# Optimization experiments

Measured on AMD Instinct MI355X. Metric: run time of the kernel, lower is better.

## Reference

```python
import jax, jax.numpy as jnp
import numpy as np

N, E, F, H = 50000, 800000, 128, 128
EPS = 1e-5


def _layernorm(x, gamma, beta):
    mu = jnp.mean(x, axis=-1, keepdims=True)
    var = jnp.mean(jnp.square(x - mu), axis=-1, keepdims=True)
    return (x - mu) * jax.lax.rsqrt(var + EPS) * gamma + beta


def setup_inputs() -> dict:
    key = jax.random.key(0)
    ks = jax.random.split(key, 12)
    x = jax.random.normal(ks[0], (N, F), dtype=jnp.float32)
    edge_idx = jax.random.randint(ks[1], (2, E), 0, N, dtype=jnp.int64)
    edge_attr = jax.random.normal(ks[2], (E, H), dtype=jnp.float32)
    u = jax.random.normal(ks[3], (N, H), dtype=jnp.float32)
    # node_mlp_1 params: Linear(F+H -> H), Linear(H -> H), LayerNorm(H)
    W1a = jax.random.normal(ks[4], (F + H, H), dtype=jnp.float32) / np.sqrt(F + H)
    b1a = jnp.zeros((H,), jnp.float32)
    W2a = jax.random.normal(ks[5], (H, H), dtype=jnp.float32) / np.sqrt(H)
    b2a = jnp.zeros((H,), jnp.float32)
    g1 = jnp.ones((H,), jnp.float32)
    be1 = jnp.zeros((H,), jnp.float32)
    # node_mlp_2 params: Linear(F+2H -> H), Linear(H -> H), LayerNorm(H)
    W1b = jax.random.normal(ks[6], (F + 2 * H, H), dtype=jnp.float32) / np.sqrt(F + 2 * H)
    b1b = jnp.zeros((H,), jnp.float32)
    W2b = jax.random.normal(ks[7], (H, H), dtype=jnp.float32) / np.sqrt(H)
    b2b = jnp.zeros((H,), jnp.float32)
    g2 = jnp.ones((H,), jnp.float32)
    be2 = jnp.zeros((H,), jnp.float32)
    return dict(x=x, edge_idx=edge_idx, edge_attr=edge_attr, u=u,
                W1a=W1a, b1a=b1a, W2a=W2a, b2a=b2a, g1=g1, be1=be1,
                W1b=W1b, b1b=b1b, W2b=W2b, b2b=b2b, g2=g2, be2=be2)


def reference(x, edge_idx, edge_attr, u,
              W1a, b1a, W2a, b2a, g1, be1,
              W1b, b1b, W2b, b2b, g2, be2):
    row, col = edge_idx[0], edge_idx[1]
    # gather source nodes, concat with edge features -> [E, F+H]
    msg = jnp.concatenate([x[col], edge_attr], axis=1)
    h = jax.nn.relu(msg @ W1a + b1a)
    h = _layernorm(h @ W2a + b2a, g1, be1)  # [E, H]
    # scatter_mean over destination nodes
    summed = jax.ops.segment_sum(h, row, num_segments=x.shape[0])
    counts = jax.ops.segment_sum(jnp.ones((h.shape[0],), h.dtype), row,
                                 num_segments=x.shape[0])
    agg = summed / jnp.clip(counts, 1.0)[:, None]  # [N, H]
    z = jnp.concatenate([x, agg, u], axis=1)  # [N, F+2H]
    z = jax.nn.relu(z @ W1b + b1b)
    return _layernorm(z @ W2b + b2b, g2, be2)  # [N, H]
```

## Files before the change

kernel.cpp:

```cpp
#include <hip/hip_runtime.h>
#include <hip/hip_fp16.h>


typedef __bf16 bf16x8 __attribute__((ext_vector_type(8)));
typedef float floatx4 __attribute__((ext_vector_type(4)));

__device__ __forceinline__ unsigned short f2bf(float f) {
    unsigned int u = __float_as_uint(f);
    u = u + 0x7FFFu + ((u >> 16) & 1u);
    return (unsigned short)(u >> 16);
}
__device__ __forceinline__ unsigned int pk2(float a, float b) {
    return (unsigned int)f2bf(a) | ((unsigned int)f2bf(b) << 16);
}

__global__ void detect_idx64(const unsigned int* __restrict__ idx, int* __restrict__ flag) {
    if (threadIdx.x == 0 && blockIdx.x == 0) {
        unsigned int o = 0;
        for (int i = 1; i < 64; i += 2) o |= idx[i];
        *flag = (o == 0u) ? 1 : 0;
    }
}

__global__ void prep_weights(const float* __restrict__ W1a, const float* __restrict__ W2a,
                             const float* __restrict__ W1b, const float* __restrict__ W2b,
                             unsigned short* __restrict__ w1aT, unsigned short* __restrict__ w2aT,
                             unsigned short* __restrict__ w1bT, unsigned short* __restrict__ w2bT) {
    int g = blockIdx.x * 256 + threadIdx.x;
    if (g < 32768) {
        int n = g >> 8, k = g & 255;
        w1aT[g] = f2bf(W1a[k * 128 + n]);
    } else if (g < 49152) {
        int l = g - 32768; int n = l >> 7, k = l & 127;
        w2aT[l] = f2bf(W2a[k * 128 + n]);
    } else if (g < 98304) {
        int l = g - 49152; int n = l / 384, k = l - n * 384;
        w1bT[l] = f2bf(W1b[k * 128 + n]);
    } else if (g < 114688) {
        int l = g - 98304; int n = l >> 7, k = l & 127;
        w2bT[l] = f2bf(W2b[k * 128 + n]);
    }
}

__global__ __launch_bounds__(256, 2) void edge_mlp_scatter(
    const float* __restrict__ x, const void* __restrict__ eidx,
    const float* __restrict__ ea,
    const float* __restrict__ b1a, const float* __restrict__ b2a,
    const float* __restrict__ g1, const float* __restrict__ be1,
    const unsigned short* __restrict__ w1aT, const unsigned short* __restrict__ w2aT,
    float* __restrict__ summed, __half* __restrict__ summedH,
    float* __restrict__ counts,
    const int* __restrict__ flag64, int E, int useHalf)
{
    __shared__ union {
        unsigned short msg[64 * 264];
        float h2[64 * 132];
    } uA;
    __shared__ unsigned short h1s[64 * 136];
    __shared__ int lsRow[64], lsCol[64];
    __shared__ float sMean[64], sRstd[64];

    const int tid  = threadIdx.x;
    const int lane = tid & 63;
    const int wave = tid >> 6;
    const int quad = lane >> 4;
    const int lm   = lane & 15;
    const int ns   = wave * 32;

    bf16x8 wf1[8][2], wf2[4][2];
#pragma unroll
    for (int kk = 0; kk < 8; kk++)
#pragma unroll
        for (int nt = 0; nt < 2; nt++)
            wf1[kk][nt] = *(const bf16x8*)(w1aT + (ns + nt * 16 + lm) * 256 + kk * 32 + quad * 8);
#pragma unroll
    for (int kk = 0; kk < 4; kk++)
#pragma unroll
        for (int nt = 0; nt < 2; nt++)
            wf2[kk][nt] = *(const bf16x8*)(w2aT + (ns + nt * 16 + lm) * 128 + kk * 32 + quad * 8);

    float b1v[2], b2v[2];
#pragma unroll
    for (int nt = 0; nt < 2; nt++) {
        b1v[nt] = b1a[ns + nt * 16 + lm];
        b2v[nt] = b2a[ns + nt * 16 + lm];
    }
    const int colT = tid & 127;
    const float gv = g1[colT], bev = be1[colT];
    const int colP = tid & 63, eg4 = tid >> 6;
    float gA = 0.f, gB = 0.f, bA = 0.f, bB = 0.f;
    if (useHalf) {
        gA = g1[colP * 2];  gB = g1[colP * 2 + 1];
        bA = be1[colP * 2]; bB = be1[colP * 2 + 1];
    }
    const int use64 = *flag64;

    const int numTiles = (E + 63) >> 6;
    for (int t = blockIdx.x; t < numTiles; t += gridDim.x) {
        const int eb = t << 6;
        __syncthreads();
        if (tid < 64) {
            int e = eb + tid; if (e >= E) e = E - 1;
            int r, c;
            if (use64) { const long long* p = (const long long*)eidx; r = (int)p[e]; c = (int)p[E + e]; }
            else       { const int* p = (const int*)eidx;             r = p[e];      c = p[E + e]; }
            lsRow[tid] = r; lsCol[tid] = c;
        }
        __syncthreads();
        {
            const int rl = tid >> 5, l32 = tid & 31;
#pragma unroll
            for (int it = 0; it < 8; it++) {
                const int e = it * 8 + rl;
                int eg = eb + e; if (eg >= E) eg = E - 1;
                const float4 xv = ((const float4*)(x + (size_t)lsCol[e] * 128))[l32];
                const float4 av = ((const float4*)(ea + (size_t)eg * 128))[l32];
                *(unsigned int*)&uA.msg[e * 264 + l32 * 4]           = pk2(xv.x, xv.y);
                *(unsigned int*)&uA.msg[e * 264 + l32 * 4 + 2]       = pk2(xv.z, xv.w);
                *(unsigned int*)&uA.msg[e * 264 + 128 + l32 * 4]     = pk2(av.x, av.y);
                *(unsigned int*)&uA.msg[e * 264 + 128 + l32 * 4 + 2] = pk2(av.z, av.w);
            }
        }
        __syncthreads();
        floatx4 acc1[4][2] = {};
#pragma unroll
        for (int mt = 0; mt < 4; mt++)
#pragma unroll
            for (int kk = 0; kk < 8; kk++) {
                bf16x8 a = *(const bf16x8*)&uA.msg[(mt * 16 + lm) * 264 + kk * 32 + quad * 8];
                acc1[mt][0] = __builtin_amdgcn_mfma_f32_16x16x32_bf16(a, wf1[kk][0], acc1[mt][0], 0, 0, 0);
                acc1[mt][1] = __builtin_amdgcn_mfma_f32_16x16x32_bf16(a, wf1[kk][1], acc1[mt][1], 0, 0, 0);
            }
#pragma unroll
        for (int mt = 0; mt < 4; mt++)
#pragma unroll
            for (int nt = 0; nt < 2; nt++)
#pragma unroll
                for (int r = 0; r < 4; r++) {
                    const int row = mt * 16 + quad * 4 + r;
                    const int col = ns + nt * 16 + lm;
                    h1s[row * 136 + col] = f2bf(fmaxf(acc1[mt][nt][r] + b1v[nt], 0.f));
                }
        __syncthreads();
        floatx4 acc2[4][2] = {};
#pragma unroll
        for (int mt = 0; mt < 4; mt++)
#pragma unroll
            for (int kk = 0; kk < 4; kk++) {
                bf16x8 a = *(const bf16x8*)&h1s[(mt * 16 + lm) * 136 + kk * 32 + quad * 8];
                acc2[mt][0] = __builtin_amdgcn_mfma_f32_16x16x32_bf16(a, wf2[kk][0], acc2[mt][0], 0, 0, 0);
                acc2[mt][1] = __builtin_amdgcn_mfma_f32_16x16x32_bf16(a, wf2[kk][1], acc2[mt][1], 0, 0, 0);
            }
#pragma unroll
        for (int mt = 0; mt < 4; mt++)
#pragma unroll
            for (int nt = 0; nt < 2; nt++)
#pragma unroll
                for (int r = 0; r < 4; r++) {
                    const int row = mt * 16 + quad * 4 + r;
                    const int col = ns + nt * 16 + lm;
                    uA.h2[row * 132 + col] = acc2[mt][nt][r] + b2v[nt];
                }
        __syncthreads();
        {
            const int e = tid >> 2, q = tid & 3;
            const float4* hp = (const float4*)&uA.h2[e * 132 + q * 32];
            float s = 0.f, ss = 0.f;
#pragma unroll
            for (int i = 0; i < 8; i++) {
                float4 v = hp[i];
                s  += v.x + v.y + v.z + v.w;
                ss += v.x * v.x + v.y * v.y + v.z * v.z + v.w * v.w;
            }
            s  += __shfl_xor(s, 1);  s  += __shfl_xor(s, 2);
            ss += __shfl_xor(ss, 1); ss += __shfl_xor(ss, 2);
            if (q == 0) {
                float mean = s * (1.f / 128.f);
                float var  = ss * (1.f / 128.f) - mean * mean;
                sMean[e] = mean;
                sRstd[e] = rsqrtf(var + 1e-5f);
                if (eb + e < E) unsafeAtomicAdd(counts + lsRow[e], 1.f);
            }
        }
        __syncthreads();
        if (useHalf) {
#pragma unroll
            for (int it = 0; it < 16; it++) {
                const int e = it * 4 + eg4;
                if (eb + e < E) {
                    const float2 h = *(const float2*)&uA.h2[e * 132 + colP * 2];
                    const float m = sMean[e], rs = sRstd[e];
                    const float v0 = (h.x - m) * rs * gA + bA;
                    const float v1 = (h.y - m) * rs * gB + bB;
                    unsafeAtomicAdd((__half2*)(summedH + (size_t)lsRow[e] * 128 + colP * 2),
                                    __floats2half2_rn(v0, v1));
                }
            }
        } else {
#pragma unroll
            for (int it = 0; it < 32; it++) {
                const int e = it * 2 + (tid >> 7);
                if (eb + e < E) {
                    float v = (uA.h2[e * 132 + colT] - sMean[e]) * sRstd[e] * gv + bev;
                    unsafeAtomicAdd(summed + (size_t)lsRow[e] * 128 + colT, v);
                }
            }
        }
    }
}

__global__ __launch_bounds__(256, 2) void node_mlp(
    const float* __restrict__ x, const float* __restrict__ u,
    const float* summed, const __half* __restrict__ summedH,
    const float* __restrict__ counts,
    const float* __restrict__ b1b, const float* __restrict__ b2b,
    const float* __restrict__ g2, const float* __restrict__ be2,
    const unsigned short* __restrict__ w1bT, const unsigned short* __restrict__ w2bT,
    float* out, int NN, int useHalf)
{
    __shared__ union {
        unsigned short msg[32 * 392];
        float h2[32 * 132];
    } uA;
    __shared__ unsigned short h1s[32 * 136];
    __shared__ float sMean[32], sRstd[32];

    const int tid  = threadIdx.x;
    const int lane = tid & 63;
    const int wave = tid >> 6;
    const int quad = lane >> 4;
    const int lm   = lane & 15;
    const int ns   = wave * 32;

    bf16x8 wf1[12][2], wf2[4][2];
#pragma unroll
    for (int kk = 0; kk < 12; kk++)
#pragma unroll
        for (int nt = 0; nt < 2; nt++)
            wf1[kk][nt] = *(const bf16x8*)(w1bT + (ns + nt * 16 + lm) * 384 + kk * 32 + quad * 8);
#pragma unroll
    for (int kk = 0; kk < 4; kk++)
#pragma unroll
        for (int nt = 0; nt < 2; nt++)
            wf2[kk][nt] = *(const bf16x8*)(w2bT + (ns + nt * 16 + lm) * 128 + kk * 32 + quad * 8);

    float b1v[2], b2v[2];
#pragma unroll
    for (int nt = 0; nt < 2; nt++) {
        b1v[nt] = b1b[ns + nt * 16 + lm];
        b2v[nt] = b2b[ns + nt * 16 + lm];
    }
    const int colT = tid & 127;
    const float gv = g2[colT], bev = be2[colT];

    const int numTiles = (NN + 31) >> 5;
    for (int t = blockIdx.x; t < numTiles; t += gridDim.x) {
        const int nb = t << 5;
        __syncthreads();
        {
            const int rl = tid >> 5, l32 = tid & 31;
#pragma unroll
            for (int it = 0; it < 4; it++) {
                const int rloc = it * 8 + rl;
                int i = nb + rloc; if (i >= NN) i = NN - 1;
                const float4 xv = ((const float4*)(x + (size_t)i * 128))[l32];
                float4 sv;
                if (useHalf) {
                    const float2 rw = ((const float2*)(summedH + (size_t)i * 128))[l32];
                    const __half2 h01 = *(const __half2*)&rw.x;
                    const __half2 h23 = *(const __half2*)&rw.y;
                    const float2 a = __half22float2(h01);
                    const float2 b = __half22float2(h23);
                    sv.x = a.x; sv.y = a.y; sv.z = b.x; sv.w = b.y;
                } else {
                    sv = ((const float4*)(summed + (size_t)i * 128))[l32];
                }
                const float inv = 1.f / fmaxf(counts[i], 1.f);
                sv.x *= inv; sv.y *= inv; sv.z *= inv; sv.w *= inv;
                const float4 uv = ((const float4*)(u + (size_t)i * 128))[l32];
                *(unsigned int*)&uA.msg[rloc * 392 + l32 * 4]           = pk2(xv.x, xv.y);
                *(unsigned int*)&uA.msg[rloc * 392 + l32 * 4 + 2]       = pk2(xv.z, xv.w);
                *(unsigned int*)&uA.msg[rloc * 392 + 128 + l32 * 4]     = pk2(sv.x, sv.y);
                *(unsigned int*)&uA.msg[rloc * 392 + 128 + l32 * 4 + 2] = pk2(sv.z, sv.w);
                *(unsigned int*)&uA.msg[rloc * 392 + 256 + l32 * 4]     = pk2(uv.x, uv.y);
                *(unsigned int*)&uA.msg[rloc * 392 + 256 + l32 * 4 + 2] = pk2(uv.z, uv.w);
            }
        }
        __syncthreads();
        floatx4 acc1[2][2] = {};
#pragma unroll
        for (int mt = 0; mt < 2; mt++)
#pragma unroll
            for (int kk = 0; kk < 12; kk++) {
                bf16x8 a = *(const bf16x8*)&uA.msg[(mt * 16 + lm) * 392 + kk * 32 + quad * 8];
                acc1[mt][0] = __builtin_amdgcn_mfma_f32_16x16x32_bf16(a, wf1[kk][0], acc1[mt][0], 0, 0, 0);
                acc1[mt][1] = __builtin_amdgcn_mfma_f32_16x16x32_bf16(a, wf1[kk][1], acc1[mt][1], 0, 0, 0);
            }
#pragma unroll
        for (int mt = 0; mt < 2; mt++)
#pragma unroll
            for (int nt = 0; nt < 2; nt++)
#pragma unroll
                for (int r = 0; r < 4; r++) {
                    const int row = mt * 16 + quad * 4 + r;
                    const int col = ns + nt * 16 + lm;
                    h1s[row * 136 + col] = f2bf(fmaxf(acc1[mt][nt][r] + b1v[nt], 0.f));
                }
        __syncthreads();
        floatx4 acc2[2][2] = {};
#pragma unroll
        for (int mt = 0; mt < 2; mt++)
#pragma unroll
            for (int kk = 0; kk < 4; kk++) {
                bf16x8 a = *(const bf16x8*)&h1s[(mt * 16 + lm) * 136 + kk * 32 + quad * 8];
                acc2[mt][0] = __builtin_amdgcn_mfma_f32_16x16x32_bf16(a, wf2[kk][0], acc2[mt][0], 0, 0, 0);
                acc2[mt][1] = __builtin_amdgcn_mfma_f32_16x16x32_bf16(a, wf2[kk][1], acc2[mt][1], 0, 0, 0);
            }
#pragma unroll
        for (int mt = 0; mt < 2; mt++)
#pragma unroll
            for (int nt = 0; nt < 2; nt++)
#pragma unroll
                for (int r = 0; r < 4; r++) {
                    const int row = mt * 16 + quad * 4 + r;
                    const int col = ns + nt * 16 + lm;
                    uA.h2[row * 132 + col] = acc2[mt][nt][r] + b2v[nt];
                }
        __syncthreads();
        {
            const int e = tid >> 3, q = tid & 7;
            const float4* hp = (const float4*)&uA.h2[e * 132 + q * 16];
            float s = 0.f, ss = 0.f;
#pragma unroll
            for (int i = 0; i < 4; i++) {
                float4 v = hp[i];
                s  += v.x + v.y + v.z + v.w;
                ss += v.x * v.x + v.y * v.y + v.z * v.z + v.w * v.w;
            }
            s  += __shfl_xor(s, 1);  s  += __shfl_xor(s, 2);  s  += __shfl_xor(s, 4);
            ss += __shfl_xor(ss, 1); ss += __shfl_xor(ss, 2); ss += __shfl_xor(ss, 4);
            if (q == 0) {
                float mean = s * (1.f / 128.f);
                float var  = ss * (1.f / 128.f) - mean * mean;
                sMean[e] = mean;
                sRstd[e] = rsqrtf(var + 1e-5f);
            }
        }
        __syncthreads();
        {
            const int half = tid >> 7;
#pragma unroll
            for (int it = 0; it < 16; it++) {
                const int rloc = it * 2 + half;
                const int i = nb + rloc;
                if (i < NN) {
                    float v = (uA.h2[rloc * 132 + colT] - sMean[rloc]) * sRstd[rloc] * gv + bev;
                    out[(size_t)i * 128 + colT] = v;
                }
            }
        }
    }
}

extern "C" void kernel_launch(void* const* d_in, const int* in_sizes, int n_in,
                              void* d_out, int out_size, void* d_ws, size_t ws_size,
                              hipStream_t stream)
{
    const float* x   = (const float*)d_in[0];
    const void*  eidx = d_in[1];
    const float* ea  = (const float*)d_in[2];
    const float* u   = (const float*)d_in[3];
    const float* W1a = (const float*)d_in[4];
    const float* b1a = (const float*)d_in[5];
    const float* W2a = (const float*)d_in[6];
    const float* b2a = (const float*)d_in[7];
    const float* g1  = (const float*)d_in[8];
    const float* be1 = (const float*)d_in[9];
    const float* W1b = (const float*)d_in[10];
    const float* b1b = (const float*)d_in[11];
    const float* W2b = (const float*)d_in[12];
    const float* b2b = (const float*)d_in[13];
    const float* g2  = (const float*)d_in[14];
    const float* be2 = (const float*)d_in[15];

    const int NN = in_sizes[0] / 128;
    const int E  = in_sizes[2] / 128;

    float* counts = (float*)d_ws;
    int*   flag   = (int*)((char*)d_ws + (size_t)NN * 4);
    size_t woff   = (((size_t)NN * 4 + 4) + 15) & ~(size_t)15;
    unsigned short* w1aT = (unsigned short*)((char*)d_ws + woff);
    unsigned short* w2aT = w1aT + 128 * 256;
    unsigned short* w1bT = w2aT + 128 * 128;
    unsigned short* w2bT = w1bT + 128 * 384;
    size_t shoff  = (woff + (size_t)(128*256 + 128*128 + 128*384 + 128*128) * 2 + 255) & ~(size_t)255;
    __half* summedH = (__half*)((char*)d_ws + shoff);
    const int useHalf = (ws_size >= shoff + (size_t)NN * 128 * 2) ? 1 : 0;

    float* outf = (float*)d_out;

    if (useHalf) {
        hipMemsetAsync(summedH, 0, (size_t)NN * 128 * 2, stream);
    } else {
        hipMemsetAsync(d_out, 0, (size_t)out_size * 4, stream);
    }
    hipMemsetAsync(counts, 0, (size_t)NN * 4, stream);
    detect_idx64<<<1, 64, 0, stream>>>((const unsigned int*)eidx, flag);
    prep_weights<<<448, 256, 0, stream>>>(W1a, W2a, W1b, W2b, w1aT, w2aT, w1bT, w2bT);

    edge_mlp_scatter<<<512, 256, 0, stream>>>(x, eidx, ea, b1a, b2a, g1, be1,
                                              w1aT, w2aT, outf, summedH, counts, flag, E, useHalf);

    node_mlp<<<512, 256, 0, stream>>>(x, u, outf, summedH, counts, b1b, b2b, g2, be2,
                                      w1bT, w2bT, outf, NN, useHalf);
}
```

Before: 795.6 us.

## Double block size to 512 threads with 16 output columns per wave

Both the edge and node MLP kernels now run 512-thread blocks (8 waves), and each wave owns 16 output columns instead of 32. This halves the per-wave weight fragments and accumulators held in registers, which allows more resident waves per CU and more latency hiding for the gather and atomic scatter. The gather, layernorm reduction and scatter loops are re-indexed for the larger block. In exchange, each A-tile read from shared memory now feeds only one MFMA instead of two, so LDS traffic per MFMA doubles, and there are more waves per barrier.

```diff
diff --git a/kernel.cpp b/kernel.cpp
--- a/kernel.cpp
+++ b/kernel.cpp
@@ -42,7 +42,7 @@
     }
 }
 
-__global__ __launch_bounds__(256, 2) void edge_mlp_scatter(
+__global__ __launch_bounds__(512, 4) void edge_mlp_scatter(
     const float* __restrict__ x, const void* __restrict__ eidx,
     const float* __restrict__ ea,
     const float* __restrict__ b1a, const float* __restrict__ b2a,
@@ -65,29 +65,21 @@
     const int wave = tid >> 6;
     const int quad = lane >> 4;
     const int lm   = lane & 15;
-    const int ns   = wave * 32;
-
-    bf16x8 wf1[8][2], wf2[4][2];
+    const int ns   = wave * 16;
+
+    bf16x8 wf1[8], wf2[4];
 #pragma unroll
     for (int kk = 0; kk < 8; kk++)
-#pragma unroll
-        for (int nt = 0; nt < 2; nt++)
-            wf1[kk][nt] = *(const bf16x8*)(w1aT + (ns + nt * 16 + lm) * 256 + kk * 32 + quad * 8);
+        wf1[kk] = *(const bf16x8*)(w1aT + (ns + lm) * 256 + kk * 32 + quad * 8);
 #pragma unroll
     for (int kk = 0; kk < 4; kk++)
-#pragma unroll
-        for (int nt = 0; nt < 2; nt++)
-            wf2[kk][nt] = *(const bf16x8*)(w2aT + (ns + nt * 16 + lm) * 128 + kk * 32 + quad * 8);
-
-    float b1v[2], b2v[2];
-#pragma unroll
-    for (int nt = 0; nt < 2; nt++) {
-        b1v[nt] = b1a[ns + nt * 16 + lm];
-        b2v[nt] = b2a[ns + nt * 16 + lm];
-    }
+        wf2[kk] = *(const bf16x8*)(w2aT + (ns + lm) * 128 + kk * 32 + quad * 8);
+
+    const float b1v = b1a[ns + lm];
+    const float b2v = b2a[ns + lm];
     const int colT = tid & 127;
     const float gv = g1[colT], bev = be1[colT];
-    const int colP = tid & 63, eg4 = tid >> 6;
+    const int colP = tid & 63;
     float gA = 0.f, gB = 0.f, bA = 0.f, bB = 0.f;
     if (useHalf) {
         gA = g1[colP * 2];  gB = g1[colP * 2 + 1];
@@ -110,8 +102,8 @@
         {
             const int rl = tid >> 5, l32 = tid & 31;
 #pragma unroll
-            for (int it = 0; it < 8; it++) {
-                const int e = it * 8 + rl;
+            for (int it = 0; it < 4; it++) {
+                const int e = it * 16 + rl;
                 int eg = eb + e; if (eg >= E) eg = E - 1;
                 const float4 xv = ((const float4*)(x + (size_t)lsCol[e] * 128))[l32];
                 const float4 av = ((const float4*)(ea + (size_t)eg * 128))[l32];
@@ -122,58 +114,50 @@
             }
         }
         __syncthreads();
-        floatx4 acc1[4][2] = {};
+        floatx4 acc1[4] = {};
 #pragma unroll
         for (int mt = 0; mt < 4; mt++)
 #pragma unroll
             for (int kk = 0; kk < 8; kk++) {
                 bf16x8 a = *(const bf16x8*)&uA.msg[(mt * 16 + lm) * 264 + kk * 32 + quad * 8];
-                acc1[mt][0] = __builtin_amdgcn_mfma_f32_16x16x32_bf16(a, wf1[kk][0], acc1[mt][0], 0, 0, 0);
-                acc1[mt][1] = __builtin_amdgcn_mfma_f32_16x16x32_bf16(a, wf1[kk][1], acc1[mt][1], 0, 0, 0);
+                acc1[mt] = __builtin_amdgcn_mfma_f32_16x16x32_bf16(a, wf1[kk], acc1[mt], 0, 0, 0);
             }
 #pragma unroll
         for (int mt = 0; mt < 4; mt++)
 #pragma unroll
-            for (int nt = 0; nt < 2; nt++)
-#pragma unroll
-                for (int r = 0; r < 4; r++) {
-                    const int row = mt * 16 + quad * 4 + r;
-                    const int col = ns + nt * 16 + lm;
-                    h1s[row * 136 + col] = f2bf(fmaxf(acc1[mt][nt][r] + b1v[nt], 0.f));
-                }
-        __syncthreads();
-        floatx4 acc2[4][2] = {};
+            for (int r = 0; r < 4; r++) {
+                const int row = mt * 16 + quad * 4 + r;
+                h1s[row * 136 + ns + lm] = f2bf(fmaxf(acc1[mt][r] + b1v, 0.f));
+            }
+        __syncthreads();
+        floatx4 acc2[4] = {};
 #pragma unroll
         for (int mt = 0; mt < 4; mt++)
 #pragma unroll
             for (int kk = 0; kk < 4; kk++) {
                 bf16x8 a = *(const bf16x8*)&h1s[(mt * 16 + lm) * 136 + kk * 32 + quad * 8];
-                acc2[mt][0] = __builtin_amdgcn_mfma_f32_16x16x32_bf16(a, wf2[kk][0], acc2[mt][0], 0, 0, 0);
-                acc2[mt][1] = __builtin_amdgcn_mfma_f32_16x16x32_bf16(a, wf2[kk][1], acc2[mt][1], 0, 0, 0);
+                acc2[mt] = __builtin_amdgcn_mfma_f32_16x16x32_bf16(a, wf2[kk], acc2[mt], 0, 0, 0);
             }
 #pragma unroll
         for (int mt = 0; mt < 4; mt++)
 #pragma unroll
-            for (int nt = 0; nt < 2; nt++)
-#pragma unroll
-                for (int r = 0; r < 4; r++) {
-                    const int row = mt * 16 + quad * 4 + r;
-                    const int col = ns + nt * 16 + lm;
-                    uA.h2[row * 132 + col] = acc2[mt][nt][r] + b2v[nt];
-                }
-        __syncthreads();
-        {
-            const int e = tid >> 2, q = tid & 3;
-            const float4* hp = (const float4*)&uA.h2[e * 132 + q * 32];
+            for (int r = 0; r < 4; r++) {
+                const int row = mt * 16 + quad * 4 + r;
+                uA.h2[row * 132 + ns + lm] = acc2[mt][r] + b2v;
+            }
+        __syncthreads();
+        {
+            const int e = tid >> 3, q = tid & 7;
+            const float4* hp = (const float4*)&uA.h2[e * 132 + q * 16];
             float s = 0.f, ss = 0.f;
 #pragma unroll
-            for (int i = 0; i < 8; i++) {
+            for (int i = 0; i < 4; i++) {
                 float4 v = hp[i];
                 s  += v.x + v.y + v.z + v.w;
                 ss += v.x * v.x + v.y * v.y + v.z * v.z + v.w * v.w;
             }
-            s  += __shfl_xor(s, 1);  s  += __shfl_xor(s, 2);
-            ss += __shfl_xor(ss, 1); ss += __shfl_xor(ss, 2);
+            s  += __shfl_xor(s, 1);  s  += __shfl_xor(s, 2);  s  += __shfl_xor(s, 4);
+            ss += __shfl_xor(ss, 1); ss += __shfl_xor(ss, 2); ss += __shfl_xor(ss, 4);
             if (q == 0) {
                 float mean = s * (1.f / 128.f);
                 float var  = ss * (1.f / 128.f) - mean * mean;
@@ -185,8 +169,8 @@
         __syncthreads();
         if (useHalf) {
 #pragma unroll
-            for (int it = 0; it < 16; it++) {
-                const int e = it * 4 + eg4;
+            for (int it = 0; it < 8; it++) {
+                const int e = it * 8 + wave;
                 if (eb + e < E) {
                     const float2 h = *(const float2*)&uA.h2[e * 132 + colP * 2];
                     const float m = sMean[e], rs = sRstd[e];
@@ -198,8 +182,8 @@
             }
         } else {
 #pragma unroll
-            for (int it = 0; it < 32; it++) {
-                const int e = it * 2 + (tid >> 7);
+            for (int it = 0; it < 16; it++) {
+                const int e = it * 4 + (tid >> 7);
                 if (eb + e < E) {
                     float v = (uA.h2[e * 132 + colT] - sMean[e]) * sRstd[e] * gv + bev;
                     unsafeAtomicAdd(summed + (size_t)lsRow[e] * 128 + colT, v);
@@ -209,7 +193,7 @@
     }
 }
 
-__global__ __launch_bounds__(256, 2) void node_mlp(
+__global__ __launch_bounds__(512, 4) void node_mlp(
     const float* __restrict__ x, const float* __restrict__ u,
     const float* summed, const __half* __restrict__ summedH,
     const float* __restrict__ counts,
@@ -230,26 +214,18 @@
     const int wave = tid >> 6;
     const int quad = lane >> 4;
     const int lm   = lane & 15;
-    const int ns   = wave * 32;
-
-    bf16x8 wf1[12][2], wf2[4][2];
+    const int ns   = wave * 16;
+
+    bf16x8 wf1[12], wf2[4];
 #pragma unroll
     for (int kk = 0; kk < 12; kk++)
-#pragma unroll
-        for (int nt = 0; nt < 2; nt++)
-            wf1[kk][nt] = *(const bf16x8*)(w1bT + (ns + nt * 16 + lm) * 384 + kk * 32 + quad * 8);
+        wf1[kk] = *(const bf16x8*)(w1bT + (ns + lm) * 384 + kk * 32 + quad * 8);
 #pragma unroll
     for (int kk = 0; kk < 4; kk++)
-#pragma unroll
-        for (int nt = 0; nt < 2; nt++)
-            wf2[kk][nt] = *(const bf16x8*)(w2bT + (ns + nt * 16 + lm) * 128 + kk * 32 + quad * 8);
-
-    float b1v[2], b2v[2];
-#pragma unroll
-    for (int nt = 0; nt < 2; nt++) {
-        b1v[nt] = b1b[ns + nt * 16 + lm];
-        b2v[nt] = b2b[ns + nt * 16 + lm];
-    }
+        wf2[kk] = *(const bf16x8*)(w2bT + (ns + lm) * 128 + kk * 32 + quad * 8);
+
+    const float b1v = b1b[ns + lm];
+    const float b2v = b2b[ns + lm];
     const int colT = tid & 127;
     const float gv = g2[colT], bev = be2[colT];
 
@@ -260,8 +236,8 @@
         {
             const int rl = tid >> 5, l32 = tid & 31;
 #pragma unroll
-            for (int it = 0; it < 4; it++) {
-                const int rloc = it * 8 + rl;
+            for (int it = 0; it < 2; it++) {
+                const int rloc = it * 16 + rl;
                 int i = nb + rloc; if (i >= NN) i = NN - 1;
                 const float4 xv = ((const float4*)(x + (size_t)i * 128))[l32];
                 float4 sv;
@@ -287,58 +263,50 @@
             }
         }
         __syncthreads();
-        floatx4 acc1[2][2] = {};
+        floatx4 acc1[2] = {};
 #pragma unroll
         for (int mt = 0; mt < 2; mt++)
 #pragma unroll
             for (int kk = 0; kk < 12; kk++) {
                 bf16x8 a = *(const bf16x8*)&uA.msg[(mt * 16 + lm) * 392 + kk * 32 + quad * 8];
-                acc1[mt][0] = __builtin_amdgcn_mfma_f32_16x16x32_bf16(a, wf1[kk][0], acc1[mt][0], 0, 0, 0);
-                acc1[mt][1] = __builtin_amdgcn_mfma_f32_16x16x32_bf16(a, wf1[kk][1], acc1[mt][1], 0, 0, 0);
+                acc1[mt] = __builtin_amdgcn_mfma_f32_16x16x32_bf16(a, wf1[kk], acc1[mt], 0, 0, 0);
             }
 #pragma unroll
         for (int mt = 0; mt < 2; mt++)
 #pragma unroll
-            for (int nt = 0; nt < 2; nt++)
-#pragma unroll
-                for (int r = 0; r < 4; r++) {
-                    const int row = mt * 16 + quad * 4 + r;
-                    const int col = ns + nt * 16 + lm;
-                    h1s[row * 136 + col] = f2bf(fmaxf(acc1[mt][nt][r] + b1v[nt], 0.f));
-                }
-        __syncthreads();
-        floatx4 acc2[2][2] = {};
+            for (int r = 0; r < 4; r++) {
+                const int row = mt * 16 + quad * 4 + r;
+                h1s[row * 136 + ns + lm] = f2bf(fmaxf(acc1[mt][r] + b1v, 0.f));
+            }
+        __syncthreads();
+        floatx4 acc2[2] = {};
 #pragma unroll
         for (int mt = 0; mt < 2; mt++)
 #pragma unroll
             for (int kk = 0; kk < 4; kk++) {
                 bf16x8 a = *(const bf16x8*)&h1s[(mt * 16 + lm) * 136 + kk * 32 + quad * 8];
-                acc2[mt][0] = __builtin_amdgcn_mfma_f32_16x16x32_bf16(a, wf2[kk][0], acc2[mt][0], 0, 0, 0);
-                acc2[mt][1] = __builtin_amdgcn_mfma_f32_16x16x32_bf16(a, wf2[kk][1], acc2[mt][1], 0, 0, 0);
+                acc2[mt] = __builtin_amdgcn_mfma_f32_16x16x32_bf16(a, wf2[kk], acc2[mt], 0, 0, 0);
             }
 #pragma unroll
         for (int mt = 0; mt < 2; mt++)
 #pragma unroll
-            for (int nt = 0; nt < 2; nt++)
-#pragma unroll
-                for (int r = 0; r < 4; r++) {
-                    const int row = mt * 16 + quad * 4 + r;
-                    const int col = ns + nt * 16 + lm;
-                    uA.h2[row * 132 + col] = acc2[mt][nt][r] + b2v[nt];
-                }
-        __syncthreads();
-        {
-            const int e = tid >> 3, q = tid & 7;
-            const float4* hp = (const float4*)&uA.h2[e * 132 + q * 16];
+            for (int r = 0; r < 4; r++) {
+                const int row = mt * 16 + quad * 4 + r;
+                uA.h2[row * 132 + ns + lm] = acc2[mt][r] + b2v;
+            }
+        __syncthreads();
+        {
+            const int e = tid >> 4, q = tid & 15;
+            const float4* hp = (const float4*)&uA.h2[e * 132 + q * 8];
             float s = 0.f, ss = 0.f;
 #pragma unroll
-            for (int i = 0; i < 4; i++) {
+            for (int i = 0; i < 2; i++) {
                 float4 v = hp[i];
                 s  += v.x + v.y + v.z + v.w;
                 ss += v.x * v.x + v.y * v.y + v.z * v.z + v.w * v.w;
             }
-            s  += __shfl_xor(s, 1);  s  += __shfl_xor(s, 2);  s  += __shfl_xor(s, 4);
-            ss += __shfl_xor(ss, 1); ss += __shfl_xor(ss, 2); ss += __shfl_xor(ss, 4);
+            s  += __shfl_xor(s, 1);  s  += __shfl_xor(s, 2);  s  += __shfl_xor(s, 4);  s  += __shfl_xor(s, 8);
+            ss += __shfl_xor(ss, 1); ss += __shfl_xor(ss, 2); ss += __shfl_xor(ss, 4); ss += __shfl_xor(ss, 8);
             if (q == 0) {
                 float mean = s * (1.f / 128.f);
                 float var  = ss * (1.f / 128.f) - mean * mean;
@@ -348,10 +316,10 @@
         }
         __syncthreads();
         {
-            const int half = tid >> 7;
-#pragma unroll
-            for (int it = 0; it < 16; it++) {
-                const int rloc = it * 2 + half;
+            const int g4 = tid >> 7;
+#pragma unroll
+            for (int it = 0; it < 8; it++) {
+                const int rloc = it * 4 + g4;
                 const int i = nb + rloc;
                 if (i < NN) {
                     float v = (uA.h2[rloc * 132 + colT] - sMean[rloc]) * sRstd[rloc] * gv + bev;
@@ -408,9 +376,9 @@
     detect_idx64<<<1, 64, 0, stream>>>((const unsigned int*)eidx, flag);
     prep_weights<<<448, 256, 0, stream>>>(W1a, W2a, W1b, W2b, w1aT, w2aT, w1bT, w2bT);
 
-    edge_mlp_scatter<<<512, 256, 0, stream>>>(x, eidx, ea, b1a, b2a, g1, be1,
+    edge_mlp_scatter<<<512, 512, 0, stream>>>(x, eidx, ea, b1a, b2a, g1, be1,
                                               w1aT, w2aT, outf, summedH, counts, flag, E, useHalf);
 
-    node_mlp<<<512, 256, 0, stream>>>(x, u, outf, summedH, counts, b1b, b2b, g2, be2,
+    node_mlp<<<512, 512, 0, stream>>>(x, u, outf, summedH, counts, b1b, b2b, g2, be2,
                                       w1bT, w2bT, outf, NN, useHalf);
 }
```

Measured after the change: 904.6 us. 13.7% more time.
